# Optimization experiments

Hardware: AMD Instinct MI355X
Metric: run time of the kernel (lower is better)

## Reference

```python
import jax, jax.numpy as jnp
import numpy as np

MODES = 2
LC = 4
N = 6000
KNN = 10
NODES = 64
CH = MODES ** 2
M = N * 2 * (KNN + 1)  # total candidate couplings


def setup_inputs() -> dict:
    key = jax.random.key(0)
    ks = jax.random.split(key, 6)
    return {
        "CK_inputs": jax.random.normal(ks[0], (N, 2 * (KNN + 1), 3), dtype=jnp.float32),
        "W_in": jax.random.normal(ks[1], (3, NODES), dtype=jnp.float32) * 0.1,
        "b_in": jnp.zeros((NODES,), dtype=jnp.float32),
        "W_hid": jax.random.normal(ks[2], (LC - 1, NODES, NODES), dtype=jnp.float32) * 0.1,
        "b_hid": jnp.zeros((LC - 1, NODES), dtype=jnp.float32),
        "W_out": jax.random.normal(ks[3], (NODES, CH), dtype=jnp.float32) * 0.1,
        "b_out": jnp.zeros((CH,), dtype=jnp.float32),
        "coo": jax.random.randint(ks[4], (2, M), 0, N, dtype=jnp.int32),
    }


def _mlp(x, W_in, b_in, W_hid, b_hid, W_out, b_out):
    # MLP: 3 -> 64, (LC-1) hidden 64->64 layers, 64 -> CH; ReLU activations.
    h = jax.nn.relu(x @ W_in + b_in)
    for i in range(W_hid.shape[0]):  # small fixed layer count
        h = jax.nn.relu(h @ W_hid[i] + b_hid[i])
    return h @ W_out + b_out  # [M, CH]


def reference(CK_inputs, W_in, b_in, W_hid, b_hid, W_out, b_out, coo):
    C_stripped = _mlp(CK_inputs.reshape(-1, 3), W_in, b_in, W_hid, b_hid, W_out, b_out)  # [M, CH]
    D = MODES * N
    # Original: for channel ch = mi*MODES+mj, scatter C_stripped[:, ch] at indices coo*MODES+mj
    # (mj added to BOTH row and col, replicating the source exactly). Indices are
    # independent of mi, so sum over mi first, then one scatter-add per mj.
    vals = C_stripped.reshape(-1, MODES, MODES).sum(axis=1)  # [M, MODES]; axis1=mi, axis2=mj
    dense = jnp.zeros((D, D), dtype=CK_inputs.dtype)
    for mj in range(MODES):
        idx = coo * MODES + mj  # [2, M]
        dense = dense.at[idx[0], idx[1]].add(vals[:, mj])
    return dense
```

## Files before the change

kernel.cpp:

```cpp
#include <hip/hip_runtime.h>
#include <stdint.h>

#define NN    6000
#define KNNC  10
#define MM    (NN * 2 * (KNNC + 1))
#define DD    (2 * NN)
#define LCH   3
#define BLK   256

#define RB        128
#define RPL       2
#define MLPGRID   ((MM + RB - 1) / RB)
#define OUTBYTES  ((size_t)DD * DD * 4)

__global__ __launch_bounds__(BLK, 4) void mlp_scatter(
    const float* __restrict__ CK,
    const float* __restrict__ Win,
    const float* __restrict__ bin,
    const float* __restrict__ Whid,
    const float* __restrict__ bhid,
    const float* __restrict__ Wout,
    const float* __restrict__ bout,
    const int* __restrict__ coo,
    float* __restrict__ out)
{
    __shared__ float sH[64 * RB];

    const int tid  = threadIdx.x;
    const int wave = tid >> 6;
    const int lane = tid & 63;
    const int jo = __builtin_amdgcn_readfirstlane((tid >> 6) << 4);

    const int rbase = blockIdx.x * RB;
    const int mb0   = rbase + lane * 2;
    const int mb    = mb0 < MM ? mb0 : MM - 2;

    const float2 ca = *(const float2*)(CK + mb * 3);
    const float2 cb = *(const float2*)(CK + mb * 3 + 2);
    const float2 cc = *(const float2*)(CK + mb * 3 + 4);
    const float x0[RPL] = {ca.x, cb.y};
    const float x1[RPL] = {ca.y, cc.x};
    const float x2[RPL] = {cb.x, cc.y};

#pragma unroll
    for (int jj = 0; jj < 16; jj++) {
        const int j = jo + jj;
        const float w0 = Win[j], w1 = Win[64 + j], w2 = Win[128 + j];
        const float bj = bin[j];
        float2 hv;
        hv.x = fmaxf(fmaf(x2[0], w2, fmaf(x1[0], w1, fmaf(x0[0], w0, bj))), 0.f);
        hv.y = fmaxf(fmaf(x2[1], w2, fmaf(x1[1], w1, fmaf(x0[1], w0, bj))), 0.f);
        *(float2*)(sH + j * RB + lane * 2) = hv;
    }
    __syncthreads();

#pragma unroll 1
    for (int l = 0; l < LCH; l++) {
        const float* __restrict__ Wl = Whid + (l << 12) + jo;
        const float* __restrict__ bh = bhid + (l << 6) + jo;

        float g[RPL][16];
#pragma unroll
        for (int jj = 0; jj < 16; jj++) {
            const float bj = bh[jj];
            g[0][jj] = bj;
            g[1][jj] = bj;
        }

#pragma unroll 4
        for (int k = 0; k < 64; k++) {
            const float4 wa = *(const float4*)(Wl + (k << 6));
            const float4 wb = *(const float4*)(Wl + (k << 6) + 4);
            const float4 wc = *(const float4*)(Wl + (k << 6) + 8);
            const float4 wd = *(const float4*)(Wl + (k << 6) + 12);
            const float2 hv = *(const float2*)(sH + k * RB + lane * 2);
            const float hk[RPL] = {hv.x, hv.y};
#pragma unroll
            for (int r = 0; r < RPL; r++) {
                g[r][0]  = fmaf(wa.x, hk[r], g[r][0]);
                g[r][1]  = fmaf(wa.y, hk[r], g[r][1]);
                g[r][2]  = fmaf(wa.z, hk[r], g[r][2]);
                g[r][3]  = fmaf(wa.w, hk[r], g[r][3]);
                g[r][4]  = fmaf(wb.x, hk[r], g[r][4]);
                g[r][5]  = fmaf(wb.y, hk[r], g[r][5]);
                g[r][6]  = fmaf(wb.z, hk[r], g[r][6]);
                g[r][7]  = fmaf(wb.w, hk[r], g[r][7]);
                g[r][8]  = fmaf(wc.x, hk[r], g[r][8]);
                g[r][9]  = fmaf(wc.y, hk[r], g[r][9]);
                g[r][10] = fmaf(wc.z, hk[r], g[r][10]);
                g[r][11] = fmaf(wc.w, hk[r], g[r][11]);
                g[r][12] = fmaf(wd.x, hk[r], g[r][12]);
                g[r][13] = fmaf(wd.y, hk[r], g[r][13]);
                g[r][14] = fmaf(wd.z, hk[r], g[r][14]);
                g[r][15] = fmaf(wd.w, hk[r], g[r][15]);
            }
        }
        __syncthreads();

#pragma unroll
        for (int jj = 0; jj < 16; jj++) {
            float2 hv;
            hv.x = fmaxf(g[0][jj], 0.f);
            hv.y = fmaxf(g[1][jj], 0.f);
            *(float2*)(sH + (jo + jj) * RB + lane * 2) = hv;
        }
        __syncthreads();
    }

    float v0[RPL], v1[RPL];
    const float b02 = bout[0] + bout[2], b13 = bout[1] + bout[3];
#pragma unroll
    for (int r = 0; r < RPL; r++) { v0[r] = b02; v1[r] = b13; }
#pragma unroll 8
    for (int k = 0; k < 64; k++) {
        const float4 wo = ((const float4*)Wout)[k];
        const float wxz = wo.x + wo.z, wyw = wo.y + wo.w;
        const float2 hv = *(const float2*)(sH + k * RB + lane * 2);
        v0[0] = fmaf(hv.x, wxz, v0[0]);  v1[0] = fmaf(hv.x, wyw, v1[0]);
        v0[1] = fmaf(hv.y, wxz, v0[1]);  v1[1] = fmaf(hv.y, wyw, v1[1]);
    }

    if (wave < 2) {
        const int mrow = mb0 + wave;
        if (mrow < MM) {
            const float sv0 = wave == 0 ? v0[0] : v0[1];
            const float sv1 = wave == 0 ? v1[0] : v1[1];
            const int r2 = coo[mrow] * 2;
            const int c2 = coo[MM + mrow] * 2;
            const long long f0i = (long long)r2 * DD + c2;
            unsafeAtomicAdd(out + f0i, sv0);
            unsafeAtomicAdd(out + f0i + DD + 1, sv1);
        }
    }
}

extern "C" void kernel_launch(void* const* d_in, const int* in_sizes, int n_in,
                              void* d_out, int out_size, void* d_ws, size_t ws_size,
                              hipStream_t stream) {
    const float* CK   = (const float*)d_in[0];
    const float* Win  = (const float*)d_in[1];
    const float* bin  = (const float*)d_in[2];
    const float* Whid = (const float*)d_in[3];
    const float* bhid = (const float*)d_in[4];
    const float* Wout = (const float*)d_in[5];
    const float* bout = (const float*)d_in[6];
    const int* coo    = (const int*)d_in[7];
    float* out        = (float*)d_out;

    hipMemsetAsync(out, 0, OUTBYTES, stream);
    mlp_scatter<<<MLPGRID, BLK, 0, stream>>>(
        CK, Win, bin, Whid, bhid, Wout, bout, coo, out);
}
```

Measured before the change: 649.0 us.

## Overlap output zero-fill with MLP compute and split scatter into separate kernel

Replaces the separate memset with a fused kernel whose blocks are interleaved: two of every three blocks zero-fill the 576MB dense output with float4 stores, and every third block runs the MLP and writes per-row values to workspace. A second kernel then performs the atomic scatter-adds. The aim is to hide the MLP compute under the bandwidth-bound fill, at the cost of an extra launch and a workspace round trip for the values.

Measured after the change: 650.2 us. Within noise of the previous version (+0.2%).

```diff
diff --git a/kernel.cpp b/kernel.cpp
--- a/kernel.cpp
+++ b/kernel.cpp
@@ -8,12 +8,15 @@
 #define LCH   3
 #define BLK   256
 
-#define RB        128
-#define RPL       2
-#define MLPGRID   ((MM + RB - 1) / RB)
-#define OUTBYTES  ((size_t)DD * DD * 4)
+#define RB     128
+#define RPL    2
+#define MLPB   1032
+#define FILLB  2064
+#define GRID   (MLPB + FILLB)
+#define NV     ((long long)DD * DD / 4)
+#define SCGRID ((MM + BLK - 1) / BLK)
 
-__global__ __launch_bounds__(BLK, 4) void mlp_scatter(
+__global__ __launch_bounds__(BLK, 4) void fused_fill_mlp(
     const float* __restrict__ CK,
     const float* __restrict__ Win,
     const float* __restrict__ bin,
@@ -21,17 +24,29 @@
     const float* __restrict__ bhid,
     const float* __restrict__ Wout,
     const float* __restrict__ bout,
-    const int* __restrict__ coo,
+    float* __restrict__ vals,
     float* __restrict__ out)
 {
     __shared__ float sH[64 * RB];
 
-    const int tid  = threadIdx.x;
+    const int bid = blockIdx.x;
+    const int tid = threadIdx.x;
+
+    if (bid % 3 != 2) {
+        const int fid = (bid / 3) * 2 + (bid % 3);
+        long long i = (long long)fid * BLK + tid;
+        const long long stride = (long long)FILLB * BLK;
+        float4 z = make_float4(0.f, 0.f, 0.f, 0.f);
+        float4* outv = (float4*)out;
+        for (; i < NV; i += stride) outv[i] = z;
+        return;
+    }
+
     const int wave = tid >> 6;
     const int lane = tid & 63;
     const int jo = __builtin_amdgcn_readfirstlane((tid >> 6) << 4);
 
-    const int rbase = blockIdx.x * RB;
+    const int rbase = (bid / 3) * RB;
     const int mb0   = rbase + lane * 2;
     const int mb    = mb0 < MM ? mb0 : MM - 2;
 
@@ -119,19 +134,24 @@
         v0[0] = fmaf(hv.x, wxz, v0[0]);  v1[0] = fmaf(hv.x, wyw, v1[0]);
         v0[1] = fmaf(hv.y, wxz, v0[1]);  v1[1] = fmaf(hv.y, wyw, v1[1]);
     }
+    if (wave == 0 && mb0 < MM) {
+        *(float4*)(vals + 2 * mb0) = make_float4(v0[0], v1[0], v0[1], v1[1]);
+    }
+}
 
-    if (wave < 2) {
-        const int mrow = mb0 + wave;
-        if (mrow < MM) {
-            const float sv0 = wave == 0 ? v0[0] : v0[1];
-            const float sv1 = wave == 0 ? v1[0] : v1[1];
-            const int r2 = coo[mrow] * 2;
-            const int c2 = coo[MM + mrow] * 2;
-            const long long f0i = (long long)r2 * DD + c2;
-            unsafeAtomicAdd(out + f0i, sv0);
-            unsafeAtomicAdd(out + f0i + DD + 1, sv1);
-        }
-    }
+__global__ __launch_bounds__(BLK) void scatter_add(
+    const float* __restrict__ vals,
+    const int* __restrict__ coo,
+    float* __restrict__ out)
+{
+    const int t = blockIdx.x * BLK + threadIdx.x;
+    if (t >= MM) return;
+    const int r2 = coo[t] * 2;
+    const int c2 = coo[MM + t] * 2;
+    const float2 v = *(const float2*)(vals + 2 * t);
+    const long long f0 = (long long)r2 * DD + c2;
+    unsafeAtomicAdd(out + f0, v.x);
+    unsafeAtomicAdd(out + f0 + DD + 1, v.y);
 }
 
 extern "C" void kernel_launch(void* const* d_in, const int* in_sizes, int n_in,
@@ -146,8 +166,9 @@
     const float* bout = (const float*)d_in[6];
     const int* coo    = (const int*)d_in[7];
     float* out        = (float*)d_out;
+    float* vals       = (float*)d_ws;
 
-    hipMemsetAsync(out, 0, OUTBYTES, stream);
-    mlp_scatter<<<MLPGRID, BLK, 0, stream>>>(
-        CK, Win, bin, Whid, bhid, Wout, bout, coo, out);
+    fused_fill_mlp<<<GRID, BLK, 0, stream>>>(
+        CK, Win, bin, Whid, bhid, Wout, bout, vals, out);
+    scatter_add<<<SCGRID, BLK, 0, stream>>>(vals, coo, out);
 }
```
